# Kernel optimization log

Hardware: AMD Instinct MI355X
Metric: run time of the kernel (lower is better)

Reference implementation:

```python
import jax, jax.numpy as jnp
import numpy as np
from jax.scipy.special import logsumexp

K, V, D, R, S_ITERS = 512, 50257, 300, 75, 20


def setup_inputs() -> dict:
    key = jax.random.key(0)
    ks = jax.random.split(key, 4)
    word_embeds = jax.random.normal(ks[0], (V, D), dtype=jnp.float32)  # frozen GloVe table
    anchors = jax.random.normal(ks[1], (K, D), dtype=jnp.float32) * 0.02
    M_U = jax.random.normal(ks[2], (D, R), dtype=jnp.float32) * (1.0 / D ** 0.5)
    # word_proj initialized to identity in torch (nn.init.eye_); add tiny noise to avoid degeneracy
    Wp = jnp.eye(D, dtype=jnp.float32) + 0.01 * jax.random.normal(ks[3], (D, D), dtype=jnp.float32)
    log_eps = jnp.float32(-2.3)
    topic_scale = jnp.ones((K, 1), dtype=jnp.float32)
    return {"word_embeds": word_embeds, "anchors": anchors, "M_U": M_U,
            "Wp": Wp, "log_eps": log_eps, "topic_scale": topic_scale}


def _l2norm(x):
    # F.normalize(dim=-1) with eps clamp
    n = jnp.maximum(jnp.linalg.norm(x, axis=-1, keepdims=True), 1e-12)
    return x / n


def reference(word_embeds, anchors, M_U, Wp, log_eps, topic_scale):
    # torch Linear: x @ W.T
    w = _l2norm(word_embeds @ Wp.T)   # [V, d]
    a = _l2norm(anchors)              # [K, d]

    # Mahalanobis cost with M = I + U U^T
    M = jnp.eye(D, dtype=w.dtype) + M_U @ M_U.T    # [d, d]
    MA = a @ M                                      # [K, d]
    MW = w @ M                                      # [V, d]
    AA = jnp.sum(MA * a, axis=-1)                   # [K]
    WW = jnp.sum(MW * w, axis=-1)                   # [V]
    cost = jnp.maximum(AA[:, None] + WW[None, :] - 2.0 * (MA @ w.T), 0.0)  # [K, V]

    eps = jax.nn.softplus(log_eps) + 1e-4
    log_kern = -cost / eps                          # [K, V]

    # 20-step log-domain Sinkhorn
    def body(carry, _):
        log_u, log_v = carry
        log_u = -logsumexp(log_kern + log_v, axis=1, keepdims=True)  # [K, 1]
        log_v = -logsumexp(log_kern + log_u, axis=0, keepdims=True)  # [1, V]
        return (log_u, log_v), None

    init = (jnp.zeros((K, 1), log_kern.dtype), jnp.zeros((1, V), log_kern.dtype))
    (log_u, log_v), _ = jax.lax.scan(body, init, None, length=S_ITERS)

    log_P = log_kern + log_u + log_v
    log_beta = log_P - logsumexp(log_P, axis=1, keepdims=True)
    beta = jnp.exp(log_beta) * jax.nn.softplus(topic_scale)
    beta = beta / jnp.sum(beta, axis=1, keepdims=True)
    return beta  # [K, V]
```

## Files before the change

### kernel.cpp

```cpp
#include <hip/hip_runtime.h>
#include <math.h>

#define KT 512
#define VW 50257
#define DD 300
#define RR 75
#define DR 375
#define GAMMA 0.010187536f
#define NB 786
#define SLOTS 8

typedef _Float16 half8 __attribute__((ext_vector_type(8)));
typedef float f32x4 __attribute__((ext_vector_type(4)));
typedef float f4a __attribute__((ext_vector_type(4), aligned(4)));

__device__ __forceinline__ void load_lds16(const void* g, void* l) {
  __builtin_amdgcn_global_load_lds(
      (const __attribute__((address_space(1))) unsigned int*)g,
      (__attribute__((address_space(3))) unsigned int*)l, 16, 0, 0);
}

__device__ inline float block_reduce_sum(float val, float* sbuf) {
  int t = threadIdx.x;
  sbuf[t] = val;
  __syncthreads();
  for (int off = blockDim.x >> 1; off > 0; off >>= 1) {
    if (t < off) sbuf[t] += sbuf[t + off];
    __syncthreads();
  }
  float r = sbuf[0];
  __syncthreads();
  return r;
}

template <int CTRL>
__device__ __forceinline__ float dpp_add_step(float x) {
  int yi = __builtin_amdgcn_update_dpp(0, __float_as_int(x), CTRL, 0xf, 0xf, false);
  return x + __int_as_float(yi);
}
__device__ __forceinline__ float row16_reduce_add(float x) {
  x = dpp_add_step<0x111>(x);
  x = dpp_add_step<0x112>(x);
  x = dpp_add_step<0x114>(x);
  x = dpp_add_step<0x118>(x);
  return x;
}

__global__ void prep_We_split(const float* __restrict__ We, _Float16* __restrict__ We2) {
  int v = blockIdx.x, c = threadIdx.x;
  float x = (c < DD) ? We[(size_t)v * DD + c] : 0.f;
  _Float16 h = (_Float16)x;
  We2[(size_t)v * 640 + c] = h;
  We2[(size_t)v * 640 + 320 + c] = (_Float16)(x - (float)h);
}

__global__ void prep_bext(const float* __restrict__ Wp, const float* __restrict__ MU,
                          float* __restrict__ Bext) {
  int id = blockIdx.x * blockDim.x + threadIdx.x;
  if (id >= DR * DD) return;
  int row = id / DD, d = id - row * DD;
  if (row < DD) {
    Bext[id] = Wp[row * DD + d];
  } else {
    int r = row - DD;
    float s = 0.f;
    for (int j = 0; j < DD; ++j) s += MU[j * RR + r] * Wp[j * DD + d];
    Bext[id] = s;
  }
}

__global__ void prep_bext_split(const float* __restrict__ BextR, _Float16* __restrict__ Bext2) {
  int r = blockIdx.x, c = threadIdx.x;
  float x = (r < DR && c < DD) ? BextR[r * DD + c] : 0.f;
  _Float16 h = (_Float16)x;
  Bext2[(size_t)r * 640 + c] = h;
  Bext2[(size_t)r * 640 + 320 + c] = (_Float16)(x - (float)h);
}

__global__ void prep_anchors(const float* __restrict__ anchors, const float* __restrict__ MU,
                             _Float16* __restrict__ Ahat2, float* __restrict__ AA) {
  __shared__ float a[DD];
  __shared__ float psh[RR];
  __shared__ float red[128];
  __shared__ float inv_sh;
  int k = blockIdx.x, t = threadIdx.x;
  float ss = 0.f;
  for (int d = t; d < DD; d += 128) {
    float x = anchors[k * DD + d];
    a[d] = x;
    ss += x * x;
  }
  ss = block_reduce_sum(ss, red);
  if (t == 0) inv_sh = 1.f / fmaxf(sqrtf(ss), 1e-12f);
  __syncthreads();
  float inv = inv_sh;
  float p2 = 0.f;
  if (t < RR) {
    float p = 0.f;
    for (int j = 0; j < DD; ++j) p += MU[j * RR + t] * a[j];
    p *= inv;
    psh[t] = p;
    p2 = p * p;
  }
  p2 = block_reduce_sum(p2, red);
  _Float16* row = Ahat2 + (size_t)k * 768;
  for (int d = t; d < 384; d += 128) {
    float val = (d < DD) ? a[d] * inv : ((d < DR) ? psh[d - DD] : 0.f);
    _Float16 h = (_Float16)val;
    row[d] = h;
    row[384 + d] = (_Float16)(val - (float)h);
  }
  if (t == 0) AA[k] = 1.f + p2;
}

__global__ void prep_words(float* __restrict__ WhatR, float* __restrict__ WW) {
  __shared__ float red[128];
  __shared__ float inv_sh;
  int v = blockIdx.x, t = threadIdx.x;
  float* rowf = WhatR + (size_t)v * 384;
  float x0 = rowf[t];
  float x1 = rowf[t + 128];
  float x2 = (t + 256 < DR) ? rowf[t + 256] : 0.f;
  float ss = x0 * x0 + x1 * x1 + ((t < 44) ? x2 * x2 : 0.f);
  ss = block_reduce_sum(ss, red);
  if (t == 0) inv_sh = 1.f / fmaxf(sqrtf(ss), 1e-12f);
  __syncthreads();
  float inv = inv_sh;
  x0 *= inv; x1 *= inv; x2 *= inv;
  float p2 = (t >= 44 && t + 256 < DR) ? x2 * x2 : 0.f;
  p2 = block_reduce_sum(p2, red);
  _Float16* rowh = (_Float16*)rowf;
  _Float16 h0 = (_Float16)x0;
  rowh[t] = h0; rowh[384 + t] = (_Float16)(x0 - (float)h0);
  _Float16 h1 = (_Float16)x1;
  rowh[128 + t] = h1; rowh[512 + t] = (_Float16)(x1 - (float)h1);
  float v2 = (t + 256 < DR) ? x2 : 0.f;
  _Float16 h2 = (_Float16)v2;
  rowh[256 + t] = h2; rowh[640 + t] = (_Float16)(v2 - (float)h2);
  if (t == 0) WW[v] = 1.f + p2;
}

template <int EPI>
__global__ __launch_bounds__(256) void gemm_mfma(
    const _Float16* __restrict__ Ag, int ldaE,
    const _Float16* __restrict__ Bg, int ldbE,
    float* __restrict__ C, long ldc,
    int M, int N, int KTOT, int SEGL, int mOnX,
    const float* __restrict__ AAv, const float* __restrict__ WWv,
    const float* __restrict__ log_eps_ptr) {
  __shared__ __align__(16) _Float16 As[2 * 128 * 64];
  __shared__ __align__(16) _Float16 Bs[2 * 128 * 64];
  int t = threadIdx.x, lane = t & 63, w = t >> 6;

  int nwg = gridDim.x * gridDim.y;
  int orig = blockIdx.y * gridDim.x + blockIdx.x;
  int q = nwg >> 3, r8 = nwg & 7;
  int xcd = orig & 7, pos = orig >> 3;
  int wgid = (xcd < r8 ? xcd * (q + 1) : r8 * (q + 1) + (xcd - r8) * q) + pos;
  int bxi = wgid % gridDim.x;
  int byi = wgid / gridDim.x;

  int bm = (mOnX ? bxi : byi) * 128;
  int bn = (mOnX ? byi : bxi) * 128;
  int wm = w >> 1, wn = w & 1;
  f32x4 acc[4][4] = {};
  size_t ldaB = (size_t)ldaE * 2, ldbB = (size_t)ldbE * 2;
  int srow = lane >> 3, sg = lane & 7;
  int lr = lane & 15, kq = lane >> 4;
  int NT = KTOT >> 6;

  auto stage = [&](int buf, int kt) {
    int k0 = kt << 6;
    int ak = (k0 >= 2 * SEGL) ? k0 - 2 * SEGL : k0;
    int bk = (k0 >= SEGL) ? k0 - SEGL : k0;
    size_t akb = (size_t)ak * 2, bkb = (size_t)bk * 2;
#pragma unroll
    for (int qq = 0; qq < 4; ++qq) {
      int iid = w * 4 + qq;
      int r = iid * 8 + srow;
      int gs = sg ^ (r & 7);
      int gmr = bm + r; if (gmr >= M) gmr = M - 1;
      load_lds16((const char*)Ag + (size_t)gmr * ldaB + akb + (gs << 4),
                 (char*)As + buf * 16384 + iid * 1024);
      int gnr = bn + r; if (gnr >= N) gnr = N - 1;
      load_lds16((const char*)Bg + (size_t)gnr * ldbB + bkb + (gs << 4),
                 (char*)Bs + buf * 16384 + iid * 1024);
    }
  };

  stage(0, 0);
  __syncthreads();
  int cur = 0;
  for (int kt = 0; kt < NT; ++kt) {
    if (kt + 1 < NT) stage(cur ^ 1, kt + 1);
    const char* Ab = (const char*)As + cur * 16384;
    const char* Bb = (const char*)Bs + cur * 16384;
#pragma unroll
    for (int ks = 0; ks < 2; ++ks) {
      half8 af[4], bf[4];
#pragma unroll
      for (int i = 0; i < 4; ++i) {
        int row = wm * 64 + i * 16 + lr;
        af[i] = *(const half8*)(Ab + row * 128 +
                                ((((ks << 2) + kq) ^ (row & 7)) << 4));
        int col = wn * 64 + i * 16 + lr;
        bf[i] = *(const half8*)(Bb + col * 128 +
                                ((((ks << 2) + kq) ^ (col & 7)) << 4));
      }
#pragma unroll
      for (int i = 0; i < 4; ++i)
#pragma unroll
        for (int j = 0; j < 4; ++j)
          acc[i][j] = __builtin_amdgcn_mfma_f32_16x16x32_f16(af[i], bf[j], acc[i][j], 0, 0, 0);
    }
    __syncthreads();
    cur ^= 1;
  }

  float s2e = 0.f;
  if (EPI == 1) {
    float le = log_eps_ptr[0];
    float eps = log1pf(__expf(le)) + 1e-4f;
    s2e = 1.4426950408889634f / eps;
  }
  int rq = lane >> 4;
#pragma unroll
  for (int i = 0; i < 4; ++i) {
#pragma unroll
    for (int j = 0; j < 4; ++j) {
#pragma unroll
      for (int r = 0; r < 4; ++r) {
        int gm = bm + wm * 64 + i * 16 + rq * 4 + r;
        int gn = bn + wn * 64 + j * 16 + lr;
        if (gm < M && gn < N) {
          float c = acc[i][j][r];
          if (EPI == 0) {
            C[(size_t)gm * ldc + gn] = c;
          } else {
            float e = exp2f((2.f * c - AAv[gm] - WWv[gn]) * s2e);
            C[(size_t)gm * ldc + gn] = fminf(e, 1.0f);
          }
        }
      }
    }
  }
}

template <int FIRST>
__global__ __launch_bounds__(512) void sweep(const float* __restrict__ E,
                                             const float* __restrict__ Sprev,
                                             float* __restrict__ Scur,
                                             float* __restrict__ vout) {
  __shared__ float u_sh[KT];
  __shared__ __align__(16) float colp[32][64];
  __shared__ __align__(16) float v_sh[64];
  __shared__ float rowacc[KT];
  int t = threadIdx.x;
  int c4 = t & 15, rg = t >> 4;
  int c0 = blockIdx.x * 64;
  int colb = c0 + c4 * 4;
  bool full = (c0 + 64 <= VW);

  float4 tl[16];
  const float* bp = E + (size_t)rg * VW + colb;
  if (full) {
#pragma unroll
    for (int j = 0; j < 16; ++j) {
      f4a x = *(const f4a*)bp;
      tl[j] = make_float4(x.x, x.y, x.z, x.w);
      bp += (size_t)32 * VW;
    }
  } else {
#pragma unroll
    for (int j = 0; j < 16; ++j) {
      float4 x;
      x.x = (colb + 0 < VW) ? bp[0] : 0.f;
      x.y = (colb + 1 < VW) ? bp[1] : 0.f;
      x.z = (colb + 2 < VW) ? bp[2] : 0.f;
      x.w = (colb + 3 < VW) ? bp[3] : 0.f;
      tl[j] = x;
      bp += (size_t)32 * VW;
    }
  }

  float4 vq;
  if (FIRST) {
    vq = make_float4(1.f, 1.f, 1.f, 1.f);
  } else {
    float s = 0.f;
#pragma unroll
    for (int q = 0; q < SLOTS; ++q) s += Sprev[q * KT + t];
    u_sh[t] = 1.0f / fmaxf(s, 1e-35f);
    __syncthreads();
    float4 cs = make_float4(0.f, 0.f, 0.f, 0.f);
#pragma unroll
    for (int j = 0; j < 16; ++j) {
      float u = u_sh[rg + 32 * j];
      cs.x = fmaf(tl[j].x, u, cs.x);
      cs.y = fmaf(tl[j].y, u, cs.y);
      cs.z = fmaf(tl[j].z, u, cs.z);
      cs.w = fmaf(tl[j].w, u, cs.w);
    }
    *(float4*)&colp[rg][c4 * 4] = cs;
    __syncthreads();
    if (t < 64) {
      float s2 = 0.f;
#pragma unroll
      for (int q = 0; q < 32; ++q) s2 += colp[q][t];
      float vv = (c0 + t < VW) ? GAMMA / fmaxf(s2, 1e-35f) : 0.f;
      v_sh[t] = vv;
      if (c0 + t < VW) vout[c0 + t] = vv;
    }
    __syncthreads();
    vq = *(const float4*)&v_sh[c4 * 4];
  }

#pragma unroll
  for (int j = 0; j < 16; ++j) {
    float x = fmaf(tl[j].x, vq.x, fmaf(tl[j].y, vq.y,
              fmaf(tl[j].z, vq.z, tl[j].w * vq.w)));
    x = row16_reduce_add(x);
    if (c4 == 15) rowacc[rg + 32 * j] = x;
  }
  __syncthreads();
  unsafeAtomicAdd(&Scur[(size_t)(blockIdx.x & (SLOTS - 1)) * KT + t], rowacc[t]);
}

__global__ __launch_bounds__(256) void write_beta(float* __restrict__ out,
                                                  const float* __restrict__ Sfin,
                                                  const float* __restrict__ vv) {
  __shared__ float uk_sh;
  int k = blockIdx.y;
  int t = threadIdx.x;
  if (t == 0) {
    float s = 0.f;
#pragma unroll
    for (int q = 0; q < SLOTS; ++q) s += Sfin[q * KT + k];
    uk_sh = 1.0f / fmaxf(s, 1e-35f);
  }
  __syncthreads();
  float uk = uk_sh;
  int v4 = (blockIdx.x * 256 + t) * 4;
  if (v4 + 4 <= VW) {
    size_t id = (size_t)k * VW + v4;
    f4a e = *(const f4a*)(out + id);
    float4 w = *(const float4*)(vv + v4);
    f4a o;
    o.x = e.x * (uk * w.x); o.y = e.y * (uk * w.y);
    o.z = e.z * (uk * w.z); o.w = e.w * (uk * w.w);
    *(f4a*)(out + id) = o;
  } else {
#pragma unroll
    for (int j = 0; j < 4; ++j) {
      if (v4 + j < VW) {
        size_t id = (size_t)k * VW + v4 + j;
        out[id] = out[id] * (uk * vv[v4 + j]);
      }
    }
  }
}

extern "C" void kernel_launch(void* const* d_in, const int* in_sizes, int n_in,
                              void* d_out, int out_size, void* d_ws, size_t ws_size,
                              hipStream_t stream) {
  const float* We = (const float*)d_in[0];
  const float* An = (const float*)d_in[1];
  const float* MU = (const float*)d_in[2];
  const float* Wp = (const float*)d_in[3];
  const float* log_eps = (const float*)d_in[4];
  float* out = (float*)d_out;

  char* p = (char*)d_ws;
  auto take = [&](size_t b) { char* r = p; p += (b + 255) & ~(size_t)255; return r; };
  _Float16* We2   = (_Float16*)take((size_t)VW * 640 * 2);
  _Float16* Bext2 = (_Float16*)take((size_t)384 * 640 * 2);
  _Float16* Ahat2 = (_Float16*)take((size_t)KT * 768 * 2);
  float* WhatR    = (float*)take((size_t)VW * 384 * 4);
  float* BextR    = (float*)take((size_t)DR * DD * 4);
  float* AA       = (float*)take(KT * 4);
  float* WW       = (float*)take((size_t)VW * 4);
  float* Sbuf     = (float*)take((size_t)21 * SLOTS * KT * 4);
  float* VVb      = (float*)take((size_t)VW * 4);
  _Float16* What2 = (_Float16*)WhatR;

  (void)hipMemsetAsync(Sbuf, 0, (size_t)21 * SLOTS * KT * 4, stream);

  prep_We_split<<<VW, 320, 0, stream>>>(We, We2);
  prep_bext<<<(DR * DD + 255) / 256, 256, 0, stream>>>(Wp, MU, BextR);
  prep_bext_split<<<384, 320, 0, stream>>>(BextR, Bext2);
  prep_anchors<<<KT, 128, 0, stream>>>(An, MU, Ahat2, AA);

  gemm_mfma<0><<<dim3(3, 393), 256, 0, stream>>>(
      We2, 640, Bext2, 640, WhatR, 384, VW, 384, 960, 320, 0,
      nullptr, nullptr, nullptr);

  prep_words<<<VW, 128, 0, stream>>>(WhatR, WW);

  gemm_mfma<1><<<dim3(4, 393), 256, 0, stream>>>(
      Ahat2, 768, What2, 768, out, VW, KT, VW, 1152, 384, 1,
      AA, WW, log_eps);

  sweep<1><<<NB, 512, 0, stream>>>(out, nullptr, Sbuf, nullptr);
  for (int s = 1; s <= 20; ++s) {
    sweep<0><<<NB, 512, 0, stream>>>(out, Sbuf + (size_t)(s - 1) * SLOTS * KT,
                                     Sbuf + (size_t)s * SLOTS * KT, VVb);
  }

  dim3 g3((VW + 1023) / 1024, KT);
  write_beta<<<g3, 256, 0, stream>>>(out, Sbuf + (size_t)20 * SLOTS * KT, VVb);
}
```

Measured before the change: 862.3 us.

## Fuse first Sinkhorn row-sum into cost GEMM epilogue; widen sweep blocks

```diff
diff --git a/kernel.cpp b/kernel.cpp
--- a/kernel.cpp
+++ b/kernel.cpp
@@ -7,7 +7,7 @@
 #define RR 75
 #define DR 375
 #define GAMMA 0.010187536f
-#define NB 786
+#define NBS 393
 #define SLOTS 8
 
 typedef _Float16 half8 __attribute__((ext_vector_type(8)));
@@ -43,6 +43,11 @@
   x = dpp_add_step<0x112>(x);
   x = dpp_add_step<0x114>(x);
   x = dpp_add_step<0x118>(x);
+  return x;
+}
+__device__ __forceinline__ float row32_reduce_add(float x) {
+  x = row16_reduce_add(x);
+  x = dpp_add_step<0x142>(x);
   return x;
 }
 
@@ -147,9 +152,10 @@
     float* __restrict__ C, long ldc,
     int M, int N, int KTOT, int SEGL, int mOnX,
     const float* __restrict__ AAv, const float* __restrict__ WWv,
-    const float* __restrict__ log_eps_ptr) {
-  __shared__ __align__(16) _Float16 As[2 * 128 * 64];
-  __shared__ __align__(16) _Float16 Bs[2 * 128 * 64];
+    const float* __restrict__ log_eps_ptr, float* __restrict__ Sb0) {
+  __shared__ __align__(16) _Float16 As[128 * 64];
+  __shared__ __align__(16) _Float16 Bs[128 * 64];
+  __shared__ float epart[128][2];
   int t = threadIdx.x, lane = t & 63, w = t >> 6;
 
   int nwg = gridDim.x * gridDim.y;
@@ -167,10 +173,8 @@
   size_t ldaB = (size_t)ldaE * 2, ldbB = (size_t)ldbE * 2;
   int srow = lane >> 3, sg = lane & 7;
   int lr = lane & 15, kq = lane >> 4;
-  int NT = KTOT >> 6;
-
-  auto stage = [&](int buf, int kt) {
-    int k0 = kt << 6;
+
+  for (int k0 = 0; k0 < KTOT; k0 += 64) {
     int ak = (k0 >= 2 * SEGL) ? k0 - 2 * SEGL : k0;
     int bk = (k0 >= SEGL) ? k0 - SEGL : k0;
     size_t akb = (size_t)ak * 2, bkb = (size_t)bk * 2;
@@ -181,30 +185,22 @@
       int gs = sg ^ (r & 7);
       int gmr = bm + r; if (gmr >= M) gmr = M - 1;
       load_lds16((const char*)Ag + (size_t)gmr * ldaB + akb + (gs << 4),
-                 (char*)As + buf * 16384 + iid * 1024);
+                 (char*)As + iid * 1024);
       int gnr = bn + r; if (gnr >= N) gnr = N - 1;
       load_lds16((const char*)Bg + (size_t)gnr * ldbB + bkb + (gs << 4),
-                 (char*)Bs + buf * 16384 + iid * 1024);
-    }
-  };
-
-  stage(0, 0);
-  __syncthreads();
-  int cur = 0;
-  for (int kt = 0; kt < NT; ++kt) {
-    if (kt + 1 < NT) stage(cur ^ 1, kt + 1);
-    const char* Ab = (const char*)As + cur * 16384;
-    const char* Bb = (const char*)Bs + cur * 16384;
+                 (char*)Bs + iid * 1024);
+    }
+    __syncthreads();
 #pragma unroll
     for (int ks = 0; ks < 2; ++ks) {
       half8 af[4], bf[4];
 #pragma unroll
       for (int i = 0; i < 4; ++i) {
         int row = wm * 64 + i * 16 + lr;
-        af[i] = *(const half8*)(Ab + row * 128 +
+        af[i] = *(const half8*)((const char*)As + row * 128 +
                                 ((((ks << 2) + kq) ^ (row & 7)) << 4));
         int col = wn * 64 + i * 16 + lr;
-        bf[i] = *(const half8*)(Bb + col * 128 +
+        bf[i] = *(const half8*)((const char*)Bs + col * 128 +
                                 ((((ks << 2) + kq) ^ (col & 7)) << 4));
       }
 #pragma unroll
@@ -214,7 +210,6 @@
           acc[i][j] = __builtin_amdgcn_mfma_f32_16x16x32_f16(af[i], bf[j], acc[i][j], 0, 0, 0);
     }
     __syncthreads();
-    cur ^= 1;
   }
 
   float s2e = 0.f;
@@ -227,39 +222,59 @@
 #pragma unroll
   for (int i = 0; i < 4; ++i) {
 #pragma unroll
-    for (int j = 0; j < 4; ++j) {
-#pragma unroll
-      for (int r = 0; r < 4; ++r) {
-        int gm = bm + wm * 64 + i * 16 + rq * 4 + r;
+    for (int r = 0; r < 4; ++r) {
+      int gm = bm + wm * 64 + i * 16 + rq * 4 + r;
+      float se = 0.f;
+#pragma unroll
+      for (int j = 0; j < 4; ++j) {
         int gn = bn + wn * 64 + j * 16 + lr;
-        if (gm < M && gn < N) {
-          float c = acc[i][j][r];
-          if (EPI == 0) {
-            C[(size_t)gm * ldc + gn] = c;
-          } else {
-            float e = exp2f((2.f * c - AAv[gm] - WWv[gn]) * s2e);
-            C[(size_t)gm * ldc + gn] = fminf(e, 1.0f);
-          }
+        float c = acc[i][j][r];
+        if (EPI == 0) {
+          if (gm < M && gn < N) C[(size_t)gm * ldc + gn] = c;
+        } else {
+          float e = exp2f((2.f * c - AAv[gm < M ? gm : 0] -
+                           WWv[gn < N ? gn : 0]) * s2e);
+          e = fminf(e, 1.0f);
+          if (gn >= N) e = 0.f;
+          if (gm < M && gn < N) C[(size_t)gm * ldc + gn] = e;
+          se += e;
         }
       }
-    }
-  }
-}
-
-template <int FIRST>
-__global__ __launch_bounds__(512) void sweep(const float* __restrict__ E,
-                                             const float* __restrict__ Sprev,
-                                             float* __restrict__ Scur,
-                                             float* __restrict__ vout) {
+      if (EPI == 1) {
+        se = row16_reduce_add(se);
+        if (lr == 15) epart[wm * 64 + i * 16 + rq * 4 + r][wn] = se;
+      }
+    }
+  }
+  if (EPI == 1) {
+    __syncthreads();
+    if (t < 128) {
+      int slot = wgid & (SLOTS - 1);
+      unsafeAtomicAdd(&Sb0[(size_t)slot * KT + bm + t], epart[t][0] + epart[t][1]);
+    }
+  }
+}
+
+__global__ __launch_bounds__(1024) void sweep(const float* __restrict__ E,
+                                              const float* __restrict__ Sprev,
+                                              float* __restrict__ Scur,
+                                              float* __restrict__ vout) {
   __shared__ float u_sh[KT];
-  __shared__ __align__(16) float colp[32][64];
-  __shared__ __align__(16) float v_sh[64];
+  __shared__ __align__(16) float colp[32][128];
+  __shared__ __align__(16) float v_sh[128];
   __shared__ float rowacc[KT];
   int t = threadIdx.x;
-  int c4 = t & 15, rg = t >> 4;
-  int c0 = blockIdx.x * 64;
+  int c4 = t & 31, rg = t >> 5;
+  int c0 = blockIdx.x * 128;
   int colb = c0 + c4 * 4;
-  bool full = (c0 + 64 <= VW);
+  bool full = (c0 + 128 <= VW);
+
+  if (t < KT) {
+    float s = 0.f;
+#pragma unroll
+    for (int q = 0; q < SLOTS; ++q) s += Sprev[q * KT + t];
+    u_sh[t] = 1.0f / fmaxf(s, 1e-35f);
+  }
 
   float4 tl[16];
   const float* bp = E + (size_t)rg * VW + colb;
@@ -282,48 +297,40 @@
       bp += (size_t)32 * VW;
     }
   }
-
-  float4 vq;
-  if (FIRST) {
-    vq = make_float4(1.f, 1.f, 1.f, 1.f);
-  } else {
-    float s = 0.f;
-#pragma unroll
-    for (int q = 0; q < SLOTS; ++q) s += Sprev[q * KT + t];
-    u_sh[t] = 1.0f / fmaxf(s, 1e-35f);
-    __syncthreads();
-    float4 cs = make_float4(0.f, 0.f, 0.f, 0.f);
-#pragma unroll
-    for (int j = 0; j < 16; ++j) {
-      float u = u_sh[rg + 32 * j];
-      cs.x = fmaf(tl[j].x, u, cs.x);
-      cs.y = fmaf(tl[j].y, u, cs.y);
-      cs.z = fmaf(tl[j].z, u, cs.z);
-      cs.w = fmaf(tl[j].w, u, cs.w);
-    }
-    *(float4*)&colp[rg][c4 * 4] = cs;
-    __syncthreads();
-    if (t < 64) {
-      float s2 = 0.f;
-#pragma unroll
-      for (int q = 0; q < 32; ++q) s2 += colp[q][t];
-      float vv = (c0 + t < VW) ? GAMMA / fmaxf(s2, 1e-35f) : 0.f;
-      v_sh[t] = vv;
-      if (c0 + t < VW) vout[c0 + t] = vv;
-    }
-    __syncthreads();
-    vq = *(const float4*)&v_sh[c4 * 4];
-  }
+  __syncthreads();
+
+  float4 cs = make_float4(0.f, 0.f, 0.f, 0.f);
+#pragma unroll
+  for (int j = 0; j < 16; ++j) {
+    float u = u_sh[rg + 32 * j];
+    cs.x = fmaf(tl[j].x, u, cs.x);
+    cs.y = fmaf(tl[j].y, u, cs.y);
+    cs.z = fmaf(tl[j].z, u, cs.z);
+    cs.w = fmaf(tl[j].w, u, cs.w);
+  }
+  *(float4*)&colp[rg][c4 * 4] = cs;
+  __syncthreads();
+  if (t < 128) {
+    float s2 = 0.f;
+#pragma unroll
+    for (int q = 0; q < 32; ++q) s2 += colp[q][t];
+    float vv = (c0 + t < VW) ? GAMMA / fmaxf(s2, 1e-35f) : 0.f;
+    v_sh[t] = vv;
+    if (c0 + t < VW) vout[c0 + t] = vv;
+  }
+  __syncthreads();
+  float4 vq = *(const float4*)&v_sh[c4 * 4];
 
 #pragma unroll
   for (int j = 0; j < 16; ++j) {
     float x = fmaf(tl[j].x, vq.x, fmaf(tl[j].y, vq.y,
               fmaf(tl[j].z, vq.z, tl[j].w * vq.w)));
-    x = row16_reduce_add(x);
-    if (c4 == 15) rowacc[rg + 32 * j] = x;
-  }
-  __syncthreads();
-  unsafeAtomicAdd(&Scur[(size_t)(blockIdx.x & (SLOTS - 1)) * KT + t], rowacc[t]);
+    x = row32_reduce_add(x);
+    if ((t & 31) == 31) rowacc[rg + 32 * j] = x;
+  }
+  __syncthreads();
+  if (t < KT)
+    unsafeAtomicAdd(&Scur[(size_t)(blockIdx.x & (SLOTS - 1)) * KT + t], rowacc[t]);
 }
 
 __global__ __launch_bounds__(256) void write_beta(float* __restrict__ out,
@@ -392,18 +399,17 @@
 
   gemm_mfma<0><<<dim3(3, 393), 256, 0, stream>>>(
       We2, 640, Bext2, 640, WhatR, 384, VW, 384, 960, 320, 0,
-      nullptr, nullptr, nullptr);
+      nullptr, nullptr, nullptr, nullptr);
 
   prep_words<<<VW, 128, 0, stream>>>(WhatR, WW);
 
   gemm_mfma<1><<<dim3(4, 393), 256, 0, stream>>>(
       Ahat2, 768, What2, 768, out, VW, KT, VW, 1152, 384, 1,
-      AA, WW, log_eps);
-
-  sweep<1><<<NB, 512, 0, stream>>>(out, nullptr, Sbuf, nullptr);
+      AA, WW, log_eps, Sbuf);
+
   for (int s = 1; s <= 20; ++s) {
-    sweep<0><<<NB, 512, 0, stream>>>(out, Sbuf + (size_t)(s - 1) * SLOTS * KT,
-                                     Sbuf + (size_t)s * SLOTS * KT, VVb);
+    sweep<<<NBS, 1024, 0, stream>>>(out, Sbuf + (size_t)(s - 1) * SLOTS * KT,
+                                    Sbuf + (size_t)s * SLOTS * KT, VVb);
   }
 
   dim3 g3((VW + 1023) / 1024, KT);
```

Measured after the change: 854.4 us. Within noise of the previous version (-0.9%).
